# Optimization experiments

Hardware: AMD Instinct MI355X
Metric: run time of the kernel (lower is better)

The kernel has to match this reference:

```python
import jax, jax.numpy as jnp
import numpy as np

BN_EPS = 1e-5
TAU = 1.0

def _conv(x, w, pad, groups=1):
    return jax.lax.conv_general_dilated(
        x, w, (1, 1), [(pad, pad), (pad, pad)],
        feature_group_count=groups,
        dimension_numbers=('NCHW', 'OIHW', 'NCHW'))

def _bn(x, p):
    # p: (4, C) rows = gamma, beta, running_mean, running_var (eval-mode BN)
    g, b, m, v = p[0], p[1], p[2], p[3]
    scale = g * jax.lax.rsqrt(v + BN_EPS)
    shift = b - m * scale
    return x * scale[None, :, None, None] + shift[None, :, None, None]

def _dsconv(x, dw, bn1, pw, bn2, pad):
    c = x.shape[1]
    h = jax.nn.silu(_bn(_conv(x, dw, pad, groups=c), bn1))
    return jax.nn.silu(_bn(_conv(h, pw, 0), bn2))

def _make_bn(key, ch):
    k1, k2, k3, k4 = jax.random.split(key, 4)
    g = 1.0 + 0.1 * jax.random.normal(k1, (ch,), jnp.float32)
    b = 0.1 * jax.random.normal(k2, (ch,), jnp.float32)
    m = 0.1 * jax.random.normal(k3, (ch,), jnp.float32)
    v = 0.5 + jax.random.uniform(k4, (ch,), jnp.float32)
    return jnp.stack([g, b, m, v])

def setup_inputs() -> dict:
    key = jax.random.key(0)
    ks = jax.random.split(key, 18)
    B, C, H, W = 4, 256, 128, 128
    P, K = 64, 8
    inp = {
        'x':      jax.random.normal(ks[0], (B, C, H, W), jnp.float32),
        'fp_w1':  0.05 * jax.random.normal(ks[1], (P, C, 1, 1), jnp.float32),
        'fp_bn1': _make_bn(ks[2], P),
        'fp_dw':  0.2 * jax.random.normal(ks[3], (P, 1, 3, 3), jnp.float32),
        'fp_bn2': _make_bn(ks[4], P),
        'protos': jax.random.normal(ks[5], (K, P), jnp.float32),
        'bs_dw':  0.2 * jax.random.normal(ks[6], (1, 1, 3, 3), jnp.float32),
        'bs_bn1': _make_bn(ks[7], 1),
        'bs_pw':  0.2 * jax.random.normal(ks[8], (8, 1, 1, 1), jnp.float32),
        'bs_bn2': _make_bn(ks[9], 8),
        'bl_dw':  0.2 * jax.random.normal(ks[10], (1, 1, 5, 5), jnp.float32),
        'bl_bn1': _make_bn(ks[11], 1),
        'bl_pw':  0.2 * jax.random.normal(ks[12], (8, 1, 1, 1), jnp.float32),
        'bl_bn2': _make_bn(ks[13], 8),
        'fuse_w': 0.2 * jax.random.normal(ks[14], (1, 16, 1, 1), jnp.float32),
        'fuse_b': 0.1 * jax.random.normal(ks[15], (1,), jnp.float32),
        'gamma':  0.5 * jax.random.normal(ks[16], (1,), jnp.float32),
    }
    return inp

def reference(x, fp_w1, fp_bn1, fp_dw, fp_bn2, protos,
              bs_dw, bs_bn1, bs_pw, bs_bn2,
              bl_dw, bl_bn1, bl_pw, bl_bn2,
              fuse_w, fuse_b, gamma):
    # feature_proj: 1x1 conv -> BN -> SiLU -> depthwise 3x3 -> BN -> SiLU
    h = jax.nn.silu(_bn(_conv(x, fp_w1, 0), fp_bn1))
    proj = jax.nn.silu(_bn(_conv(h, fp_dw, 1, groups=fp_dw.shape[0]), fp_bn2))

    # deviation: min L2 distance to K bg prototypes, per-image min-max normalized
    B, P, H, W = proj.shape
    feat = proj.reshape(B, P, H * W).transpose(0, 2, 1)      # (B, HW, P)
    d2 = ((feat * feat).sum(-1, keepdims=True)               # (B, HW, 1)
          + (protos * protos).sum(-1)                        # (K,)
          - 2.0 * jnp.einsum('bnp,kp->bnk', feat, protos))   # (B, HW, K)
    dist = jnp.sqrt(jnp.maximum(d2, 0.0))
    min_dist = dist.min(axis=2) / (TAU + 1e-6)               # (B, HW)
    d_min = min_dist.min(axis=1, keepdims=True)
    d_max = min_dist.max(axis=1, keepdims=True)
    deviation = ((min_dist - d_min) / (d_max - d_min + 1e-6)).reshape(B, 1, H, W)

    # deviation -> attention head: two DS-conv branches (3x3 and 5x5), fuse 1x1, sigmoid
    f1 = _dsconv(deviation, bs_dw, bs_bn1, bs_pw, bs_bn2, pad=1)
    f2 = _dsconv(deviation, bl_dw, bl_bn1, bl_pw, bl_bn2, pad=2)
    attn = jax.nn.sigmoid(_conv(jnp.concatenate([f1, f2], axis=1), fuse_w, 0)
                          + fuse_b[None, :, None, None])
    return x + gamma * (x * attn)
```

## Files before the change

### kernel.cpp

```cpp
#include <hip/hip_runtime.h>
#include <math.h>

#define C_IN 256
#define P_CH 64
#define H_IMG 128
#define W_IMG 128
#define HW (H_IMG*W_IMG)
#define N_IMG 4
#define K_PROTO 8
#define BN_EPS 1e-5f

typedef unsigned short u16;
typedef __attribute__((ext_vector_type(4))) short bf16x4;
typedef __attribute__((ext_vector_type(8))) short bf16x8;
typedef __attribute__((ext_vector_type(4))) float f32x4;

#define OFF_WTBF   0
#define OFF_BIASA  8192
#define OFF_PNORM  8256
#define OFF_MINMAX 8264
#define OFF_H      8272
#define OFF_MD     (8272 + 2097152)
#define OFF_ATTN   (OFF_MD + 65536)

__device__ __forceinline__ float silu_f(float x) { return x / (1.f + __expf(-x)); }

__device__ __forceinline__ u16 f2bf(float f) {
    union { float f; unsigned u; } v; v.f = f;
    unsigned r = v.u + 0x7fffu + ((v.u >> 16) & 1u);
    return (u16)(r >> 16);
}
__device__ __forceinline__ float bf2f(u16 s) {
    union { unsigned u; float f; } v; v.u = ((unsigned)s) << 16; return v.f;
}

__global__ void prep_kernel(const float* __restrict__ w1, const float* __restrict__ bn1,
                            const float* __restrict__ protos, float* __restrict__ ws)
{
    int bx = blockIdx.x, tid = threadIdx.x;
    if (bx < 64) {
        int idx = bx * 256 + tid;
        int n = idx >> 8, k = idx & 255;
        float sc = bn1[n] * rsqrtf(bn1[192 + n] + BN_EPS);
        ((u16*)(ws + OFF_WTBF))[idx] = f2bf(w1[n * C_IN + k] * sc);
    } else {
        if (tid < 64) {
            float sc = bn1[tid] * rsqrtf(bn1[192 + tid] + BN_EPS);
            ws[OFF_BIASA + tid] = bn1[64 + tid] - bn1[128 + tid] * sc;
        }
        if (tid < 8) {
            float s = 0.f;
            for (int p = 0; p < 64; ++p) { float v = protos[tid * 64 + p]; s += v * v; }
            ws[OFF_PNORM + tid] = s;
        }
        if (tid < 4) {
            unsigned* mm = (unsigned*)(ws + OFF_MINMAX);
            mm[tid * 2]     = 0x7f7fffffu;
            mm[tid * 2 + 1] = 0u;
        }
    }
}

#define LDA 36
#define LDB 264
__global__ __launch_bounds__(256) void conv1x1_kernel(
    const float* __restrict__ x, const u16* __restrict__ wtb,
    const float* __restrict__ bias, u16* __restrict__ h)
{
    __shared__ u16 As[2][128 * LDA];
    __shared__ u16 Bs[64 * LDB];
    int bx = blockIdx.x;
    int img = bx >> 7, row = bx & 127;
    int tid = threadIdx.x;
    int wid = tid >> 6, lane = tid & 63;
    int mm = lane & 15, kb = lane >> 4;

    {
        int n = tid >> 2, k0 = (tid & 3) * 64;
        const u16* src = wtb + n * 256 + k0;
        u16* dst = Bs + n * LDB + k0;
#pragma unroll
        for (int i = 0; i < 64; i += 4)
            *(ushort4*)(dst + i) = *(const ushort4*)(src + i);
    }

    int cp = tid >> 4, pg = tid & 15;
    const float* xbase = x + (size_t)img * C_IN * HW + row * W_IMG;
    {
        const float* xc0 = xbase + (size_t)(2 * cp) * HW;
        const float* xc1 = xc0 + HW;
#pragma unroll
        for (int i = 0; i < 8; ++i) {
            int px = pg + 16 * i;
            ushort2 pk; pk.x = f2bf(xc0[px]); pk.y = f2bf(xc1[px]);
            *(ushort2*)(&As[0][px * LDA + 2 * cp]) = pk;
        }
    }
    __syncthreads();

    f32x4 acc[2][4];
#pragma unroll
    for (int mt = 0; mt < 2; ++mt)
#pragma unroll
        for (int nt = 0; nt < 4; ++nt) acc[mt][nt] = (f32x4){0.f, 0.f, 0.f, 0.f};

    for (int k = 0; k < 8; ++k) {
        float p0[8], p1[8];
        if (k < 7) {
            const float* xc0 = xbase + (size_t)((k + 1) * 32 + 2 * cp) * HW;
            const float* xc1 = xc0 + HW;
#pragma unroll
            for (int i = 0; i < 8; ++i) {
                int px = pg + 16 * i;
                p0[i] = xc0[px]; p1[i] = xc1[px];
            }
        }

        const u16* Ab = As[k & 1];
        bf16x8 afrag[2], bfrag[4];
#pragma unroll
        for (int mt = 0; mt < 2; ++mt) {
            const u16* ap = Ab + (wid * 32 + mt * 16 + mm) * LDA + kb * 8;
            bf16x4 lo = *(const bf16x4*)ap;
            bf16x4 hi = *(const bf16x4*)(ap + 4);
            afrag[mt] = __builtin_shufflevector(lo, hi, 0, 1, 2, 3, 4, 5, 6, 7);
        }
#pragma unroll
        for (int nt = 0; nt < 4; ++nt)
            bfrag[nt] = *(const bf16x8*)(Bs + (nt * 16 + mm) * LDB + k * 32 + kb * 8);
#pragma unroll
        for (int mt = 0; mt < 2; ++mt)
#pragma unroll
            for (int nt = 0; nt < 4; ++nt)
                acc[mt][nt] = __builtin_amdgcn_mfma_f32_16x16x32_bf16(
                    afrag[mt], bfrag[nt], acc[mt][nt], 0, 0, 0);

        if (k < 7) {
            u16* An = As[(k + 1) & 1];
#pragma unroll
            for (int i = 0; i < 8; ++i) {
                int px = pg + 16 * i;
                ushort2 pk; pk.x = f2bf(p0[i]); pk.y = f2bf(p1[i]);
                *(ushort2*)(&An[px * LDA + 2 * cp]) = pk;
            }
        }
        __syncthreads();
    }

#pragma unroll
    for (int mt = 0; mt < 2; ++mt) {
        int pxb = wid * 32 + mt * 16 + kb * 4;
#pragma unroll
        for (int nt = 0; nt < 4; ++nt) {
            int n = nt * 16 + mm;
            float bb = bias[n];
            ushort4 o;
            o.x = f2bf(silu_f(acc[mt][nt][0] + bb));
            o.y = f2bf(silu_f(acc[mt][nt][1] + bb));
            o.z = f2bf(silu_f(acc[mt][nt][2] + bb));
            o.w = f2bf(silu_f(acc[mt][nt][3] + bb));
            *(ushort4*)(h + ((size_t)img * P_CH + n) * HW + row * W_IMG + pxb) = o;
        }
    }
}

__global__ __launch_bounds__(1024) void dwconv_dev_kernel(
    const u16* __restrict__ h, const float* __restrict__ dw,
    const float* __restrict__ bn2, const float* __restrict__ protos,
    const float* __restrict__ pnorm, float* __restrict__ md,
    unsigned* __restrict__ minmax)
{
    __shared__ float smem[4 * 8 * 324];
    int img = blockIdx.x >> 6;
    int t = blockIdx.x & 63;
    int y0 = (t >> 3) << 4, x0 = (t & 7) << 4;
    int tid = threadIdx.x;
    int q = tid >> 8;
    int qtid = tid & 255;
    int ty = qtid >> 4, tx = qtid & 15;

    const u16* himg = h + (size_t)img * P_CH * HW;
    float* qt = smem + q * (8 * 324);

    int  pre_off[11];
    bool pre_ok[11];
    bool pre_v[11];
#pragma unroll
    for (int r = 0; r < 11; ++r) {
        int l = qtid + r * 256;
        bool valid = l < 2592;
        int cl = l / 324;
        int rr = l - cl * 324;
        int ly = rr / 18, lx = rr - ly * 18;
        int yy = y0 - 1 + ly, xx = x0 - 1 + lx;
        bool inb = (yy >= 0) & (yy < H_IMG) & (xx >= 0) & (xx < W_IMG);
        pre_v[r] = valid;
        pre_ok[r] = valid && inb;
        pre_off[r] = cl * HW + (inb ? (yy * W_IMG + xx) : 0);
    }

    float norm2 = 0.f;
    float dot[K_PROTO];
#pragma unroll
    for (int k = 0; k < K_PROTO; ++k) dot[k] = 0.f;

    {
        const u16* hs = himg + (size_t)(q * 16) * HW;
#pragma unroll
        for (int r = 0; r < 11; ++r) {
            float v = pre_ok[r] ? bf2f(hs[pre_off[r]]) : 0.f;
            if (pre_v[r]) qt[qtid + r * 256] = v;
        }
    }
    __syncthreads();

    for (int k = 0; k < 2; ++k) {
        float pf[11];
        if (k == 0) {
            const u16* hs = himg + (size_t)(q * 16 + 8) * HW;
#pragma unroll
            for (int r = 0; r < 11; ++r)
                pf[r] = pre_ok[r] ? bf2f(hs[pre_off[r]]) : 0.f;
        }

        int c0 = q * 16 + k * 8;
#pragma unroll
        for (int cl = 0; cl < 8; ++cl) {
            int ch = c0 + cl;
            const float* tc = qt + cl * 324;
            const float* wch = dw + ch * 9;
            float s = 0.f;
#pragma unroll
            for (int dy = 0; dy < 3; ++dy)
#pragma unroll
                for (int dx = 0; dx < 3; ++dx)
                    s = fmaf(tc[(ty + dy) * 18 + tx + dx], wch[dy * 3 + dx], s);
            float g = bn2[ch], bb = bn2[64 + ch], m = bn2[128 + ch], vv = bn2[192 + ch];
            float scale = g * rsqrtf(vv + BN_EPS);
            float val = silu_f(scale * s + (bb - m * scale));
            norm2 = fmaf(val, val, norm2);
#pragma unroll
            for (int kk = 0; kk < K_PROTO; ++kk)
                dot[kk] = fmaf(val, protos[kk * 64 + ch], dot[kk]);
        }

        if (k == 0) {
            __syncthreads();
#pragma unroll
            for (int r = 0; r < 11; ++r)
                if (pre_v[r]) qt[qtid + r * 256] = pf[r];
            __syncthreads();
        }
    }
    __syncthreads();

    float* P = smem;
    {
        float* dst = P + (q * 256 + qtid) * 9;
        dst[0] = norm2;
#pragma unroll
        for (int kk = 0; kk < K_PROTO; ++kk) dst[1 + kk] = dot[kk];
    }
    __syncthreads();

    float wmin = 1e30f, wmax = -1e30f, mdv = 0.f;
    if (q == 0) {
        float n2 = 0.f, dd[K_PROTO];
#pragma unroll
        for (int kk = 0; kk < K_PROTO; ++kk) dd[kk] = 0.f;
#pragma unroll
        for (int qq = 0; qq < 4; ++qq) {
            const float* src = P + (qq * 256 + qtid) * 9;
            n2 += src[0];
#pragma unroll
            for (int kk = 0; kk < K_PROTO; ++kk) dd[kk] += src[1 + kk];
        }
        float d2min = 1e30f;
#pragma unroll
        for (int kk = 0; kk < K_PROTO; ++kk)
            d2min = fminf(d2min, n2 + pnorm[kk] - 2.f * dd[kk]);
        mdv = sqrtf(fmaxf(d2min, 0.f)) * (1.f / 1.000001f);
        md[img * HW + (y0 + ty) * W_IMG + (x0 + tx)] = mdv;
        wmin = mdv; wmax = mdv;
#pragma unroll
        for (int d = 32; d > 0; d >>= 1) {
            wmin = fminf(wmin, __shfl_xor(wmin, d));
            wmax = fmaxf(wmax, __shfl_xor(wmax, d));
        }
    }
    __syncthreads();
    if (q == 0 && (qtid & 63) == 0) {
        int wid = qtid >> 6;
        smem[wid * 2]     = wmin;
        smem[wid * 2 + 1] = wmax;
    }
    __syncthreads();
    if (tid == 0) {
        float bmin = fminf(fminf(smem[0], smem[2]), fminf(smem[4], smem[6]));
        float bmax = fmaxf(fmaxf(smem[1], smem[3]), fmaxf(smem[5], smem[7]));
        atomicMin(&minmax[img * 2],     __float_as_uint(bmin));
        atomicMax(&minmax[img * 2 + 1], __float_as_uint(bmax));
    }
}

__global__ __launch_bounds__(256) void attn_kernel(
    const float* __restrict__ md, const unsigned* __restrict__ minmax,
    const float* __restrict__ bs_dw, const float* __restrict__ bs_bn1,
    const float* __restrict__ bs_pw, const float* __restrict__ bs_bn2,
    const float* __restrict__ bl_dw, const float* __restrict__ bl_bn1,
    const float* __restrict__ bl_pw, const float* __restrict__ bl_bn2,
    const float* __restrict__ fuse_w, const float* __restrict__ fuse_b,
    float* __restrict__ attn)
{
    __shared__ float tile[20 * 20];
    int img = blockIdx.x >> 6;
    int t = blockIdx.x & 63;
    int y0 = (t >> 3) << 4, x0 = (t & 7) << 4;
    int tid = threadIdx.x;
    int ty = tid >> 4, tx = tid & 15;

    float fdmin = __uint_as_float(minmax[img * 2]);
    float fdmax = __uint_as_float(minmax[img * 2 + 1]);
    float inv = 1.f / (fdmax - fdmin + 1e-6f);

    const float* mdi = md + img * HW;
    for (int l = tid; l < 400; l += 256) {
        int ly = l / 20, lx = l - ly * 20;
        int yy = y0 - 2 + ly, xx = x0 - 2 + lx;
        float v = 0.f;
        if (yy >= 0 && yy < H_IMG && xx >= 0 && xx < W_IMG)
            v = (mdi[yy * W_IMG + xx] - fdmin) * inv;
        tile[l] = v;
    }
    __syncthreads();

    float c3 = 0.f;
#pragma unroll
    for (int dy = 0; dy < 3; ++dy)
#pragma unroll
        for (int dx = 0; dx < 3; ++dx)
            c3 = fmaf(tile[(ty + 1 + dy) * 20 + tx + 1 + dx], bs_dw[dy * 3 + dx], c3);
    float c5 = 0.f;
#pragma unroll
    for (int dy = 0; dy < 5; ++dy)
#pragma unroll
        for (int dx = 0; dx < 5; ++dx)
            c5 = fmaf(tile[(ty + dy) * 20 + tx + dx], bl_dw[dy * 5 + dx], c5);

    float s1 = bs_bn1[0] * rsqrtf(bs_bn1[3] + BN_EPS);
    float t1 = silu_f(s1 * c3 + (bs_bn1[1] - bs_bn1[2] * s1));
    float s2 = bl_bn1[0] * rsqrtf(bl_bn1[3] + BN_EPS);
    float t2 = silu_f(s2 * c5 + (bl_bn1[1] - bl_bn1[2] * s2));

    float acc = fuse_b[0];
#pragma unroll
    for (int c = 0; c < 8; ++c) {
        float scs = bs_bn2[c] * rsqrtf(bs_bn2[24 + c] + BN_EPS);
        float u1 = silu_f(scs * (bs_pw[c] * t1) + (bs_bn2[8 + c] - bs_bn2[16 + c] * scs));
        acc = fmaf(fuse_w[c], u1, acc);
        float scl = bl_bn2[c] * rsqrtf(bl_bn2[24 + c] + BN_EPS);
        float u2 = silu_f(scl * (bl_pw[c] * t2) + (bl_bn2[8 + c] - bl_bn2[16 + c] * scl));
        acc = fmaf(fuse_w[8 + c], u2, acc);
    }
    float a = 1.f / (1.f + __expf(-acc));
    attn[img * HW + (y0 + ty) * W_IMG + (x0 + tx)] = a;
}

__global__ __launch_bounds__(256) void final_kernel(
    const float* __restrict__ x, const float* __restrict__ attn,
    const float* __restrict__ gamma, float* __restrict__ out)
{
    size_t i = ((size_t)blockIdx.x * 256 + (size_t)threadIdx.x) * 4;
    float g = gamma[0];
    int b = (int)(i / ((size_t)C_IN * HW));
    int hw = (int)(i % HW);
    const float4 xv = *(const float4*)(x + i);
    const float4 av = *(const float4*)(attn + (size_t)b * HW + hw);
    float4 o;
    o.x = xv.x * (1.f + g * av.x);
    o.y = xv.y * (1.f + g * av.y);
    o.z = xv.z * (1.f + g * av.z);
    o.w = xv.w * (1.f + g * av.w);
    *(float4*)(out + i) = o;
}

extern "C" void kernel_launch(void* const* d_in, const int* in_sizes, int n_in,
                              void* d_out, int out_size, void* d_ws, size_t ws_size,
                              hipStream_t stream) {
    const float* x      = (const float*)d_in[0];
    const float* fp_w1  = (const float*)d_in[1];
    const float* fp_bn1 = (const float*)d_in[2];
    const float* fp_dw  = (const float*)d_in[3];
    const float* fp_bn2 = (const float*)d_in[4];
    const float* protos = (const float*)d_in[5];
    const float* bs_dw  = (const float*)d_in[6];
    const float* bs_bn1 = (const float*)d_in[7];
    const float* bs_pw  = (const float*)d_in[8];
    const float* bs_bn2 = (const float*)d_in[9];
    const float* bl_dw  = (const float*)d_in[10];
    const float* bl_bn1 = (const float*)d_in[11];
    const float* bl_pw  = (const float*)d_in[12];
    const float* bl_bn2 = (const float*)d_in[13];
    const float* fuse_w = (const float*)d_in[14];
    const float* fuse_b = (const float*)d_in[15];
    const float* gamma  = (const float*)d_in[16];
    float* ws  = (float*)d_ws;
    float* out = (float*)d_out;

    prep_kernel<<<65, 256, 0, stream>>>(fp_w1, fp_bn1, protos, ws);
    conv1x1_kernel<<<512, 256, 0, stream>>>(x, (const u16*)(ws + OFF_WTBF),
                                            ws + OFF_BIASA, (u16*)(ws + OFF_H));
    dwconv_dev_kernel<<<256, 1024, 0, stream>>>((const u16*)(ws + OFF_H), fp_dw, fp_bn2,
                                                protos, ws + OFF_PNORM, ws + OFF_MD,
                                                (unsigned*)(ws + OFF_MINMAX));
    attn_kernel<<<256, 256, 0, stream>>>(ws + OFF_MD, (const unsigned*)(ws + OFF_MINMAX),
                                         bs_dw, bs_bn1, bs_pw, bs_bn2,
                                         bl_dw, bl_bn1, bl_pw, bl_bn2,
                                         fuse_w, fuse_b, ws + OFF_ATTN);
    final_kernel<<<16384, 256, 0, stream>>>(x, ws + OFF_ATTN, gamma, out);
}
```

Before: 187.1 us.

## Fuse prep into consumers and attention into final scaling kernel

Drops the separate prep kernel: BN-folded bf16 weights and bias are now computed inside the conv1x1 blocks, and prototype norms inside the dwconv blocks. Global atomic min/max is replaced by per-tile partial min/max that the attention kernel reduces itself. The attention computation is merged into the final elementwise pass, so each block computes its 16x16 attention tile in shared memory and applies it to 64 channels. This cuts two launches and the attn round-trip, at the cost of redundant weight conversion and recomputing the attention tile four times per spatial tile.

```diff
diff --git a/kernel.cpp b/kernel.cpp
--- a/kernel.cpp
+++ b/kernel.cpp
@@ -15,13 +15,9 @@
 typedef __attribute__((ext_vector_type(8))) short bf16x8;
 typedef __attribute__((ext_vector_type(4))) float f32x4;
 
-#define OFF_WTBF   0
-#define OFF_BIASA  8192
-#define OFF_PNORM  8256
-#define OFF_MINMAX 8264
-#define OFF_H      8272
-#define OFF_MD     (8272 + 2097152)
-#define OFF_ATTN   (OFF_MD + 65536)
+#define OFF_H    0
+#define OFF_MD   2097152
+#define OFF_BMM  (2097152 + 65536)
 
 __device__ __forceinline__ float silu_f(float x) { return x / (1.f + __expf(-x)); }
 
@@ -34,41 +30,15 @@
     union { unsigned u; float f; } v; v.u = ((unsigned)s) << 16; return v.f;
 }
 
-__global__ void prep_kernel(const float* __restrict__ w1, const float* __restrict__ bn1,
-                            const float* __restrict__ protos, float* __restrict__ ws)
-{
-    int bx = blockIdx.x, tid = threadIdx.x;
-    if (bx < 64) {
-        int idx = bx * 256 + tid;
-        int n = idx >> 8, k = idx & 255;
-        float sc = bn1[n] * rsqrtf(bn1[192 + n] + BN_EPS);
-        ((u16*)(ws + OFF_WTBF))[idx] = f2bf(w1[n * C_IN + k] * sc);
-    } else {
-        if (tid < 64) {
-            float sc = bn1[tid] * rsqrtf(bn1[192 + tid] + BN_EPS);
-            ws[OFF_BIASA + tid] = bn1[64 + tid] - bn1[128 + tid] * sc;
-        }
-        if (tid < 8) {
-            float s = 0.f;
-            for (int p = 0; p < 64; ++p) { float v = protos[tid * 64 + p]; s += v * v; }
-            ws[OFF_PNORM + tid] = s;
-        }
-        if (tid < 4) {
-            unsigned* mm = (unsigned*)(ws + OFF_MINMAX);
-            mm[tid * 2]     = 0x7f7fffffu;
-            mm[tid * 2 + 1] = 0u;
-        }
-    }
-}
-
 #define LDA 36
 #define LDB 264
 __global__ __launch_bounds__(256) void conv1x1_kernel(
-    const float* __restrict__ x, const u16* __restrict__ wtb,
-    const float* __restrict__ bias, u16* __restrict__ h)
+    const float* __restrict__ x, const float* __restrict__ w1,
+    const float* __restrict__ bn1, u16* __restrict__ h)
 {
     __shared__ u16 As[2][128 * LDA];
     __shared__ u16 Bs[64 * LDB];
+    __shared__ float bias_s[64];
     int bx = blockIdx.x;
     int img = bx >> 7, row = bx & 127;
     int tid = threadIdx.x;
@@ -77,11 +47,18 @@
 
     {
         int n = tid >> 2, k0 = (tid & 3) * 64;
-        const u16* src = wtb + n * 256 + k0;
+        float sc = bn1[n] * rsqrtf(bn1[192 + n] + BN_EPS);
+        if ((tid & 3) == 0) bias_s[n] = bn1[64 + n] - bn1[128 + n] * sc;
+        const float* src = w1 + n * 256 + k0;
         u16* dst = Bs + n * LDB + k0;
 #pragma unroll
-        for (int i = 0; i < 64; i += 4)
-            *(ushort4*)(dst + i) = *(const ushort4*)(src + i);
+        for (int i = 0; i < 64; i += 4) {
+            float4 v = *(const float4*)(src + i);
+            ushort4 o;
+            o.x = f2bf(v.x * sc); o.y = f2bf(v.y * sc);
+            o.z = f2bf(v.z * sc); o.w = f2bf(v.w * sc);
+            *(ushort4*)(dst + i) = o;
+        }
     }
 
     int cp = tid >> 4, pg = tid & 15;
@@ -153,7 +130,7 @@
 #pragma unroll
         for (int nt = 0; nt < 4; ++nt) {
             int n = nt * 16 + mm;
-            float bb = bias[n];
+            float bb = bias_s[n];
             ushort4 o;
             o.x = f2bf(silu_f(acc[mt][nt][0] + bb));
             o.y = f2bf(silu_f(acc[mt][nt][1] + bb));
@@ -167,10 +144,10 @@
 __global__ __launch_bounds__(1024) void dwconv_dev_kernel(
     const u16* __restrict__ h, const float* __restrict__ dw,
     const float* __restrict__ bn2, const float* __restrict__ protos,
-    const float* __restrict__ pnorm, float* __restrict__ md,
-    unsigned* __restrict__ minmax)
+    float* __restrict__ md, float* __restrict__ bmm)
 {
     __shared__ float smem[4 * 8 * 324];
+    __shared__ float pnorm_s[K_PROTO];
     int img = blockIdx.x >> 6;
     int t = blockIdx.x & 63;
     int y0 = (t >> 3) << 4, x0 = (t & 7) << 4;
@@ -178,6 +155,17 @@
     int q = tid >> 8;
     int qtid = tid & 255;
     int ty = qtid >> 4, tx = qtid & 15;
+
+    if (tid < K_PROTO) {
+        const float4* pr = (const float4*)(protos + tid * 64);
+        float s = 0.f;
+#pragma unroll
+        for (int i = 0; i < 16; ++i) {
+            float4 v = pr[i];
+            s += v.x * v.x + v.y * v.y + v.z * v.z + v.w * v.w;
+        }
+        pnorm_s[tid] = s;
+    }
 
     const u16* himg = h + (size_t)img * P_CH * HW;
     float* qt = smem + q * (8 * 324);
@@ -278,7 +266,7 @@
         float d2min = 1e30f;
 #pragma unroll
         for (int kk = 0; kk < K_PROTO; ++kk)
-            d2min = fminf(d2min, n2 + pnorm[kk] - 2.f * dd[kk]);
+            d2min = fminf(d2min, n2 + pnorm_s[kk] - 2.f * dd[kk]);
         mdv = sqrtf(fmaxf(d2min, 0.f)) * (1.f / 1.000001f);
         md[img * HW + (y0 + ty) * W_IMG + (x0 + tx)] = mdv;
         wmin = mdv; wmax = mdv;
@@ -298,29 +286,46 @@
     if (tid == 0) {
         float bmin = fminf(fminf(smem[0], smem[2]), fminf(smem[4], smem[6]));
         float bmax = fmaxf(fmaxf(smem[1], smem[3]), fmaxf(smem[5], smem[7]));
-        atomicMin(&minmax[img * 2],     __float_as_uint(bmin));
-        atomicMax(&minmax[img * 2 + 1], __float_as_uint(bmax));
-    }
-}
-
-__global__ __launch_bounds__(256) void attn_kernel(
-    const float* __restrict__ md, const unsigned* __restrict__ minmax,
+        bmm[(img * 64 + t) * 2]     = bmin;
+        bmm[(img * 64 + t) * 2 + 1] = bmax;
+    }
+}
+
+__global__ __launch_bounds__(256) void attn_final_kernel(
+    const float* __restrict__ x, const float* __restrict__ md,
+    const float* __restrict__ bmm,
     const float* __restrict__ bs_dw, const float* __restrict__ bs_bn1,
     const float* __restrict__ bs_pw, const float* __restrict__ bs_bn2,
     const float* __restrict__ bl_dw, const float* __restrict__ bl_bn1,
     const float* __restrict__ bl_pw, const float* __restrict__ bl_bn2,
     const float* __restrict__ fuse_w, const float* __restrict__ fuse_b,
-    float* __restrict__ attn)
+    const float* __restrict__ gamma, float* __restrict__ out)
 {
     __shared__ float tile[20 * 20];
-    int img = blockIdx.x >> 6;
-    int t = blockIdx.x & 63;
+    __shared__ __align__(16) float attn_s[256];
+    __shared__ float mmred[2];
+    int bx = blockIdx.x;
+    int img = bx >> 8;
+    int t = (bx >> 2) & 63;
+    int cg = bx & 3;
     int y0 = (t >> 3) << 4, x0 = (t & 7) << 4;
     int tid = threadIdx.x;
     int ty = tid >> 4, tx = tid & 15;
 
-    float fdmin = __uint_as_float(minmax[img * 2]);
-    float fdmax = __uint_as_float(minmax[img * 2 + 1]);
+    if (tid < 64) {
+        float mn = bmm[(img * 64 + tid) * 2];
+        float mx = bmm[(img * 64 + tid) * 2 + 1];
+#pragma unroll
+        for (int d = 32; d > 0; d >>= 1) {
+            mn = fminf(mn, __shfl_xor(mn, d));
+            mx = fmaxf(mx, __shfl_xor(mx, d));
+        }
+        if (tid == 0) { mmred[0] = mn; mmred[1] = mx; }
+    }
+    __syncthreads();
+
+    float fdmin = mmred[0];
+    float fdmax = mmred[1];
     float inv = 1.f / (fdmax - fdmin + 1e-6f);
 
     const float* mdi = md + img * HW;
@@ -362,26 +367,24 @@
         float u2 = silu_f(scl * (bl_pw[c] * t2) + (bl_bn2[8 + c] - bl_bn2[16 + c] * scl));
         acc = fmaf(fuse_w[8 + c], u2, acc);
     }
-    float a = 1.f / (1.f + __expf(-acc));
-    attn[img * HW + (y0 + ty) * W_IMG + (x0 + tx)] = a;
-}
-
-__global__ __launch_bounds__(256) void final_kernel(
-    const float* __restrict__ x, const float* __restrict__ attn,
-    const float* __restrict__ gamma, float* __restrict__ out)
-{
-    size_t i = ((size_t)blockIdx.x * 256 + (size_t)threadIdx.x) * 4;
+    attn_s[tid] = 1.f / (1.f + __expf(-acc));
+    __syncthreads();
+
+    int j = tid & 63, cs = tid >> 6;
+    int yy = y0 + (j >> 2), xq = x0 + (j & 3) * 4;
+    float4 am = *(const float4*)&attn_s[(j >> 2) * 16 + (j & 3) * 4];
     float g = gamma[0];
-    int b = (int)(i / ((size_t)C_IN * HW));
-    int hw = (int)(i % HW);
-    const float4 xv = *(const float4*)(x + i);
-    const float4 av = *(const float4*)(attn + (size_t)b * HW + hw);
-    float4 o;
-    o.x = xv.x * (1.f + g * av.x);
-    o.y = xv.y * (1.f + g * av.y);
-    o.z = xv.z * (1.f + g * av.z);
-    o.w = xv.w * (1.f + g * av.w);
-    *(float4*)(out + i) = o;
+    float m0 = 1.f + g * am.x, m1 = 1.f + g * am.y;
+    float m2 = 1.f + g * am.z, m3 = 1.f + g * am.w;
+    size_t base = ((size_t)(img * C_IN + cg * 64 + cs * 16)) * HW
+                + (size_t)yy * W_IMG + xq;
+#pragma unroll
+    for (int c = 0; c < 16; ++c) {
+        const float4 xv = *(const float4*)(x + base + (size_t)c * HW);
+        float4 o;
+        o.x = xv.x * m0; o.y = xv.y * m1; o.z = xv.z * m2; o.w = xv.w * m3;
+        *(float4*)(out + base + (size_t)c * HW) = o;
+    }
 }
 
 extern "C" void kernel_launch(void* const* d_in, const int* in_sizes, int n_in,
@@ -407,15 +410,11 @@
     float* ws  = (float*)d_ws;
     float* out = (float*)d_out;
 
-    prep_kernel<<<65, 256, 0, stream>>>(fp_w1, fp_bn1, protos, ws);
-    conv1x1_kernel<<<512, 256, 0, stream>>>(x, (const u16*)(ws + OFF_WTBF),
-                                            ws + OFF_BIASA, (u16*)(ws + OFF_H));
+    conv1x1_kernel<<<512, 256, 0, stream>>>(x, fp_w1, fp_bn1, (u16*)(ws + OFF_H));
     dwconv_dev_kernel<<<256, 1024, 0, stream>>>((const u16*)(ws + OFF_H), fp_dw, fp_bn2,
-                                                protos, ws + OFF_PNORM, ws + OFF_MD,
-                                                (unsigned*)(ws + OFF_MINMAX));
-    attn_kernel<<<256, 256, 0, stream>>>(ws + OFF_MD, (const unsigned*)(ws + OFF_MINMAX),
-                                         bs_dw, bs_bn1, bs_pw, bs_bn2,
-                                         bl_dw, bl_bn1, bl_pw, bl_bn2,
-                                         fuse_w, fuse_b, ws + OFF_ATTN);
-    final_kernel<<<16384, 256, 0, stream>>>(x, ws + OFF_ATTN, gamma, out);
-}
+                                                protos, ws + OFF_MD, ws + OFF_BMM);
+    attn_final_kernel<<<1024, 256, 0, stream>>>(x, ws + OFF_MD, ws + OFF_BMM,
+                                                bs_dw, bs_bn1, bs_pw, bs_bn2,
+                                                bl_dw, bl_bn1, bl_pw, bl_bn2,
+                                                fuse_w, fuse_b, gamma, out);
+}
```

After: 192.7 us. 1.03x slower.
